# Optimization experiments

Measured on AMD Instinct MI355X. Metric: run time of the kernel, lower is better.

Reference implementation:

```python
import jax, jax.numpy as jnp
import numpy as np
import math

# ---- architecture constants (from init_kwargs) ----
BOUND = 1.0
L = 6            # grid levels == number of residual SIREN layers (grid_level)
F = 2            # hash-grid features per level (feature_dims)
D = 256          # SIREN hidden width / out_dim (ffenc_dims)
T = 2 ** 19      # hash table size per level
BASE_RES = 16
SCALE = 2.0
BASE_SIGMA = 5.0
EXP_SIGMA = 2.0
W0_SIN = float(L - 1)        # sin_w0 = multires - 1
W0_HIGH = 2.0 * (L - 1)      # sin_w0_high
N = 262144

_PRIMES = jnp.array([1, 2654435761, 805459861], dtype=jnp.uint32)
_OFFS = jnp.array([[i, j, k] for i in (0, 1) for j in (0, 1) for k in (0, 1)], dtype=jnp.int32)  # [8,3]


def hash_grid_encode(pos01, table):
    """Multi-resolution hash grid (instant-NGP style). pos01 [N,3] in [0,1], table [L,T,F] -> [L,N,F]."""
    res = BASE_RES * (SCALE ** jnp.arange(L, dtype=jnp.float32))               # [L]
    p = pos01[None] * res[:, None, None]                                        # [L,N,3]
    p0 = jnp.floor(p)
    frac = p - p0                                                               # [L,N,3]
    coords = p0.astype(jnp.int32)[:, :, None, :] + _OFFS[None, None]            # [L,N,8,3]
    cu = coords.astype(jnp.uint32) * _PRIMES                                    # spatial hash
    h = (cu[..., 0] ^ cu[..., 1] ^ cu[..., 2]) % jnp.uint32(T)                  # [L,N,8]
    feats = jax.vmap(lambda t, idx: t[idx])(table, h.astype(jnp.int32))         # [L,N,8,F]
    w = jnp.prod(jnp.where(_OFFS[None, None].astype(bool),
                           frac[:, :, None, :], 1.0 - frac[:, :, None, :]), axis=-1)  # trilinear [L,N,8]
    return jnp.einsum('lnc,lncf->lnf', w, feats)                                # [L,N,F]


def setup_inputs() -> dict:
    key = jax.random.key(0)
    ks = jax.random.split(key, 9)
    in_pos = jax.random.uniform(ks[0], (N, 3), jnp.float32, -BOUND, BOUND)
    table = jax.random.uniform(ks[1], (L, T, F), jnp.float32, -1e-4, 1e-4)      # hash embeddings
    ffn_A = jax.random.normal(ks[2], (L, F, D), jnp.float32)                    # Fourier projection (buffer)
    # SIREN-style init
    W0 = jax.random.uniform(ks[3], (3, D), jnp.float32, -1.0 / 3.0, 1.0 / 3.0)  # first_layer_sine_init
    b0 = jnp.zeros((D,), jnp.float32)
    lim = math.sqrt(6.0 / D) / W0_SIN
    Ws = jax.random.uniform(ks[4], (L, D, D), jnp.float32, -lim, lim)
    bs = jnp.zeros((L, D), jnp.float32)
    Wh = jax.random.uniform(ks[5], (L, D, D), jnp.float32, -lim, lim)
    bh = jnp.zeros((L, D), jnp.float32)
    return {"in_pos": in_pos, "table": table, "ffn_A": ffn_A,
            "W0": W0, "b0": b0, "Ws": Ws, "bs": bs, "Wh": Wh, "bh": bh}


def reference(in_pos, table, ffn_A, W0, b0, Ws, bs, Wh, bh):
    x = in_pos / BOUND                                   # [-1,1] for SIREN branch
    pos01 = (in_pos + BOUND) / (2.0 * BOUND)             # [0,1] for hash grid
    grid_x = hash_grid_encode(pos01, table)              # [L,N,F]
    sigmas = BASE_SIGMA * (EXP_SIGMA ** jnp.arange(L, dtype=jnp.float32))
    A = ffn_A * sigmas[:, None, None]                    # per-level sigma scale
    grid_x = jnp.sin(jnp.einsum('lnf,lfd->lnd', grid_x, 2.0 * math.pi * A))  # [L,N,D]
    # SIREN trunk with per-layer grid residual + high-frequency accumulation
    x = jnp.sin(W0_SIN * (x @ W0 + b0))                  # layer 0
    x_out = jnp.zeros((in_pos.shape[0], D), dtype=in_pos.dtype)
    for i in range(L):                                   # fixed small layer count
        x = jnp.sin(W0_SIN * (x @ Ws[i] + bs[i]))
        x = grid_x[i] + x
        x_out = x_out + jnp.sin(W0_HIGH * (x @ Wh[i] + bh[i]))
    return x_out                                          # [N,D]
```

## Files before the change

### kernel.cpp

```cpp
#include <hip/hip_runtime.h>
#include <stdint.h>

typedef __attribute__((ext_vector_type(8))) _Float16 h8v;
typedef __attribute__((ext_vector_type(4))) float f4v;

#define NLVL 6
#define TSZ (1u << 19)

__device__ __forceinline__ float b2f(unsigned short u){
  union { unsigned int i; float f; } v; v.i = ((unsigned)u) << 16; return v.f;
}
__device__ __forceinline__ unsigned short f2b(float f){
  unsigned x = __float_as_uint(f);
  x = (x + 0x7fffu + ((x >> 16) & 1u)) >> 16;
  return (unsigned short)x;
}
__device__ __forceinline__ unsigned short f2h(float f){
  union { _Float16 h; unsigned short u; } v; v.h = (_Float16)f; return v.u;
}
__device__ __forceinline__ float ldx(const void* p, long i, int isb){
  return isb ? b2f(((const unsigned short*)p)[i]) : ((const float*)p)[i];
}

__global__ void kdetect(const unsigned short* inpos, int* flag){
  __shared__ int cnt;
  if (threadIdx.x == 0) cnt = 0;
  __syncthreads();
  float f = b2f(inpos[threadIdx.x * 2]);
  int ok = (f == f) && (fabsf(f) <= 1.0f);
  atomicAdd(&cnt, ok);
  __syncthreads();
  if (threadIdx.x == 0) *flag = (cnt >= 120);
}


__global__ void kconsts(const void* ffnA, const void* W0, const void* b0,
                        const void* bs, const void* bh, char* ws, int Npts){
  const int flag = *(const int*)ws;
  const size_t wt_off = 16 + (size_t)NLVL * Npts * 8;
  float* cst = (float*)(ws + wt_off + (size_t)12 * 65536 * 2);
  int idx = blockIdx.x * 256 + threadIdx.x;
  float v;
  if (idx < 768)        v = 5.0f  * ldx(W0, idx, flag);
  else if (idx < 1024)  v = 5.0f  * ldx(b0, idx - 768, flag);
  else if (idx < 2560)  v = 5.0f  * ldx(bs, idx - 1024, flag);
  else if (idx < 4096)  v = 10.0f * ldx(bh, idx - 2560, flag);
  else { int j = idx - 4096; int l = j >> 9;
         v = 31.415926535897932f * (float)(1 << l) * ldx(ffnA, j, flag); }
  cst[idx] = v;
}

__global__ void kwt(const void* Wsv, const void* Whv, char* ws, int Npts){
  const int flag = *(const int*)ws;
  unsigned short* wt = (unsigned short*)(ws + 16 + (size_t)NLVL * Npts * 8);
  int e = blockIdx.x * 256 + threadIdx.x;
  int wi = e >> 16, r = e & 65535, n = r >> 8, k = r & 255;
  const void* src = (wi < 6) ? Wsv : Whv;
  int m = (wi < 6) ? wi : wi - 6;
  long si = (long)m * 65536 + k * 256 + n;
  float w = flag ? b2f(((const unsigned short*)src)[si]) : ((const float*)src)[si];
  wt[e] = f2h(w);
}

__global__ void kgrid(const void* inpos, const void* tbl, char* ws, int Npts){
  const int flag = *(const int*)ws;
  float* gf = (float*)(ws + 16);
  int n = blockIdx.x * 256 + threadIdx.x;
  int l = blockIdx.y;
  long b3 = (long)n * 3;
  float x = ldx(inpos, b3 + 0, flag), y = ldx(inpos, b3 + 1, flag), z = ldx(inpos, b3 + 2, flag);
  float res = (float)(16 << l);
  float px = ((x + 1.0f) * 0.5f) * res;
  float py = ((y + 1.0f) * 0.5f) * res;
  float pz = ((z + 1.0f) * 0.5f) * res;
  float fx = floorf(px), fy = floorf(py), fz = floorf(pz);
  float rx = px - fx, ry = py - fy, rz = pz - fz;
  unsigned cx = (unsigned)(int)fx, cy = (unsigned)(int)fy, cz = (unsigned)(int)fz;
  unsigned ax0 = cx,                 ax1 = cx + 1u;
  unsigned ay0 = cy * 2654435761u,   ay1 = (cy + 1u) * 2654435761u;
  unsigned az0 = cz * 805459861u,    az1 = (cz + 1u) * 805459861u;
  float g0 = 0.f, g1 = 0.f;
  #pragma unroll
  for (int c = 0; c < 8; c++){
    unsigned h = (((c & 4) ? ax1 : ax0) ^ ((c & 2) ? ay1 : ay0) ^ ((c & 1) ? az1 : az0)) & (TSZ - 1u);
    float w = ((c & 4) ? rx : 1.0f - rx) * ((c & 2) ? ry : 1.0f - ry) * ((c & 1) ? rz : 1.0f - rz);
    long e = ((long)l * TSZ + h) * 2;
    float f0, f1;
    if (flag){
      unsigned v = *(const unsigned*)((const unsigned short*)tbl + e);
      f0 = b2f((unsigned short)(v & 0xffffu)); f1 = b2f((unsigned short)(v >> 16));
    } else {
      const float* tp = (const float*)tbl + e; f0 = tp[0]; f1 = tp[1];
    }
    g0 += w * f0; g1 += w * f1;
  }
  float2 o; o.x = g0; o.y = g1;
  *(float2*)(gf + ((long)l * Npts + n) * 2) = o;
}

__global__ __launch_bounds__(512) void kmain(const void* inpos, char* ws, void* outp, int Npts){
  __shared__ __align__(16) unsigned short Abuf[128 * 264];
  __shared__ __align__(16) unsigned short Wb[2 * 8192];
  __shared__ __align__(16) float cbuf[7680];
  float* sbs_p = cbuf;
  float* sbh_p = cbuf + 1536;
  float* a2_p  = cbuf + 3072;
  float* g_p   = cbuf + 6144;

  const int tid = threadIdx.x;
  const int flag = *(const int*)ws;
  const size_t wt_off = 16 + (size_t)NLVL * Npts * 8;
  const unsigned short* wt = (const unsigned short*)(ws + wt_off);
  const float* cst = (const float*)(ws + wt_off + (size_t)12 * 65536 * 2);
  const float* gf = (const float*)(ws + 16);
  const int r0 = blockIdx.x * 128;

  const int sn = tid >> 1, skk = (tid & 1) * 16;
  uint4 pa, pb;
  {
    const uint4* p = (const uint4*)(wt + sn * 256 + skk);
    pa = p[0]; pb = p[1];
  }
  for (int idx = tid; idx < 6144; idx += 512) cbuf[idx] = cst[1024 + idx];
  for (int idx = tid; idx < 1536; idx += 512){
    int l = idx >> 8, j = idx & 255;
    g_p[idx] = gf[(size_t)l * Npts * 2 + (size_t)r0 * 2 + j];
  }
  {
    int lr = tid >> 2, c0 = (tid & 3) * 64;
    long bb = (long)(r0 + lr) * 3;
    float p0v = ldx(inpos, bb + 0, flag), p1v = ldx(inpos, bb + 1, flag), p2v = ldx(inpos, bb + 2, flag);
    for (int j = 0; j < 64; j++){
      int d = c0 + j;
      float v = __sinf(p0v * cst[d] + p1v * cst[256 + d] + p2v * cst[512 + d] + cst[768 + d]);
      Abuf[lr * 264 + d] = f2h(v);
    }
  }
  {
    uint4* dw = (uint4*)(Wb + sn * 32 + skk);
    dw[0] = pa; dw[1] = pb;
  }
  __syncthreads();

  const int lane = tid & 63, wv = tid >> 6;
  const int q = lane >> 4, sx = lane & 15;
  const int wrow = (wv >> 2) * 64, wcol = (wv & 3) * 64;
  int aoff[4], boff[4];
  #pragma unroll
  for (int rt = 0; rt < 4; rt++) aoff[rt] = (wrow + rt * 16 + sx) * 264 + q * 8;
  #pragma unroll
  for (int ct = 0; ct < 4; ct++) boff[ct] = (wcol + ct * 16 + sx) * 32 + q * 8;

  const f4v zf = {0.f, 0.f, 0.f, 0.f};
  f4v xo[4][4];
  #pragma unroll
  for (int a = 0; a < 4; a++)
    #pragma unroll
    for (int b = 0; b < 4; b++) xo[a][b] = zf;

  int cur = 0;
  #pragma unroll 1
  for (int s = 0; s < 12; s++){
    const int li = s >> 1;
    const int wi = (s & 1) ? (6 + li) : li;
    f4v acc[4][4];
    #pragma unroll
    for (int a = 0; a < 4; a++)
      #pragma unroll
      for (int b = 0; b < 4; b++) acc[a][b] = zf;
    #pragma unroll 1
    for (int kc = 0; kc < 8; kc++){
      const bool havenext = !(s == 11 && kc == 7);
      if (havenext){
        int nwi, nkc;
        if (kc < 7){ nwi = wi; nkc = kc + 1; }
        else { int s2 = s + 1; nwi = (s2 & 1) ? (6 + (s2 >> 1)) : (s2 >> 1); nkc = 0; }
        const uint4* p = (const uint4*)(wt + nwi * 65536 + sn * 256 + nkc * 32 + skk);
        pa = p[0]; pb = p[1];
      }
      h8v bfr[4], afr[4];
      const unsigned short* wc = Wb + cur * 8192;
      #pragma unroll
      for (int ct = 0; ct < 4; ct++) bfr[ct] = *(const h8v*)(wc + boff[ct]);
      #pragma unroll
      for (int rt = 0; rt < 4; rt++) afr[rt] = *(const h8v*)(Abuf + aoff[rt] + kc * 32);
      #pragma unroll
      for (int rt = 0; rt < 4; rt++)
        #pragma unroll
        for (int ct = 0; ct < 4; ct++)
          acc[rt][ct] = __builtin_amdgcn_mfma_f32_16x16x32_f16(afr[rt], bfr[ct], acc[rt][ct], 0, 0, 0);
      if (havenext){
        uint4* dw = (uint4*)(Wb + (cur ^ 1) * 8192 + sn * 32 + skk);
        dw[0] = pa; dw[1] = pb;
      }
      __syncthreads();
      cur ^= 1;
    }
    if ((s & 1) == 0){
      #pragma unroll
      for (int ct = 0; ct < 4; ct++){
        int col = wcol + ct * 16 + sx;
        float sb = sbs_p[li * 256 + col];
        float a0 = a2_p[(li * 2 + 0) * 256 + col];
        float a1 = a2_p[(li * 2 + 1) * 256 + col];
        #pragma unroll
        for (int rt = 0; rt < 4; rt++)
          #pragma unroll
          for (int r = 0; r < 4; r++){
            int row = wrow + rt * 16 + q * 4 + r;
            float gg0 = g_p[li * 256 + row * 2], gg1 = g_p[li * 256 + row * 2 + 1];
            float v = __sinf(5.0f * acc[rt][ct][r] + sb) + __sinf(a0 * gg0 + a1 * gg1);
            Abuf[row * 264 + col] = f2h(v);
          }
      }
      __syncthreads();
    } else {
      #pragma unroll
      for (int ct = 0; ct < 4; ct++){
        int col = wcol + ct * 16 + sx;
        float sb = sbh_p[li * 256 + col];
        #pragma unroll
        for (int rt = 0; rt < 4; rt++)
          #pragma unroll
          for (int r = 0; r < 4; r++)
            xo[rt][ct][r] += __sinf(10.0f * acc[rt][ct][r] + sb);
      }
    }
  }
  if (flag){
    unsigned short* ob = (unsigned short*)outp;
    #pragma unroll
    for (int rt = 0; rt < 4; rt++)
      #pragma unroll
      for (int ct = 0; ct < 4; ct++)
        #pragma unroll
        for (int r = 0; r < 4; r++){
          long row = (long)r0 + wrow + rt * 16 + q * 4 + r;
          ob[row * 256 + (wcol + ct * 16 + sx)] = f2b(xo[rt][ct][r]);
        }
  } else {
    float* of = (float*)outp;
    #pragma unroll
    for (int rt = 0; rt < 4; rt++)
      #pragma unroll
      for (int ct = 0; ct < 4; ct++)
        #pragma unroll
        for (int r = 0; r < 4; r++){
          long row = (long)r0 + wrow + rt * 16 + q * 4 + r;
          of[row * 256 + (wcol + ct * 16 + sx)] = xo[rt][ct][r];
        }
  }
}

extern "C" void kernel_launch(void* const* d_in, const int* in_sizes, int n_in,
                              void* d_out, int out_size, void* d_ws, size_t ws_size,
                              hipStream_t stream){
  (void)n_in; (void)out_size; (void)ws_size;
  const void* inpos = d_in[0];
  const void* tbl   = d_in[1];
  const void* ffnA  = d_in[2];
  const void* W0    = d_in[3];
  const void* b0    = d_in[4];
  const void* Wsv   = d_in[5];
  const void* bsv   = d_in[6];
  const void* Whv   = d_in[7];
  const void* bhv   = d_in[8];
  int Npts = in_sizes[0] / 3;
  char* ws = (char*)d_ws;
  kdetect<<<1, 128, 0, stream>>>((const unsigned short*)inpos, (int*)d_ws);
  kconsts<<<28, 256, 0, stream>>>(ffnA, W0, b0, bsv, bhv, ws, Npts);
  kwt<<<3072, 256, 0, stream>>>(Wsv, Whv, ws, Npts);
  kgrid<<<dim3(Npts / 256, NLVL), 256, 0, stream>>>(inpos, tbl, ws, Npts);
  kmain<<<Npts / 128, 512, 0, stream>>>(inpos, ws, d_out, Npts);
}
```

Baseline: 1.197 ms.

## Load MFMA-fragment-ordered weights directly to registers, shrink tile, swizzle activations

Weights are now pre-permuted on device into per-lane MFMA fragment order, and each wave loads its B fragments straight from global memory into registers with a one-step prefetch. This drops the shared-memory weight double buffer and the barrier on every k-chunk. The block shrinks to 64 rows with 256 threads and launch bounds for three blocks per CU, and the activation tile uses an XOR swizzle instead of padding. The output accumulator is kept in packed fp16 to save registers, which costs accumulation precision over six layers. Every block now reads the full weights from global memory or L2, since nothing is shared through LDS anymore.

Result: slower. 1.582 ms (+32.1%).

```diff
diff --git a/kernel.cpp b/kernel.cpp
--- a/kernel.cpp
+++ b/kernel.cpp
@@ -2,6 +2,7 @@
 #include <stdint.h>
 
 typedef __attribute__((ext_vector_type(8))) _Float16 h8v;
+typedef __attribute__((ext_vector_type(2))) _Float16 h2v;
 typedef __attribute__((ext_vector_type(4))) float f4v;
 
 #define NLVL 6
@@ -21,6 +22,8 @@
 __device__ __forceinline__ float ldx(const void* p, long i, int isb){
   return isb ? b2f(((const unsigned short*)p)[i]) : ((const float*)p)[i];
 }
+
+#define SWZ(row,k) ((row)*256 + ((((k) >> 3) ^ ((row) & 7)) << 3) + ((k) & 7))
 
 __global__ void kdetect(const unsigned short* inpos, int* flag){
   __shared__ int cnt;
@@ -54,7 +57,15 @@
   const int flag = *(const int*)ws;
   unsigned short* wt = (unsigned short*)(ws + 16 + (size_t)NLVL * Npts * 8);
   int e = blockIdx.x * 256 + threadIdx.x;
-  int wi = e >> 16, r = e & 65535, n = r >> 8, k = r & 255;
+  int j  = e & 7;
+  int lane = (e >> 3) & 63;
+  int ct = (e >> 9) & 3;
+  int kc = (e >> 11) & 7;
+  int wv = (e >> 14) & 3;
+  int wi = e >> 16;
+  int sx = lane & 15, q = lane >> 4;
+  int n = wv * 64 + ct * 16 + sx;
+  int k = kc * 32 + q * 8 + j;
   const void* src = (wi < 6) ? Wsv : Whv;
   int m = (wi < 6) ? wi : wi - 6;
   long si = (long)m * 65536 + k * 256 + n;
@@ -98,67 +109,63 @@
   *(float2*)(gf + ((long)l * Npts + n) * 2) = o;
 }
 
-__global__ __launch_bounds__(512) void kmain(const void* inpos, char* ws, void* outp, int Npts){
-  __shared__ __align__(16) unsigned short Abuf[128 * 264];
-  __shared__ __align__(16) unsigned short Wb[2 * 8192];
-  __shared__ __align__(16) float cbuf[7680];
-  float* sbs_p = cbuf;
-  float* sbh_p = cbuf + 1536;
-  float* a2_p  = cbuf + 3072;
-  float* g_p   = cbuf + 6144;
+__global__ __launch_bounds__(256, 3) void kmain(const void* inpos, char* ws, void* outp, int Npts){
+  __shared__ __align__(16) unsigned short Abuf[64 * 256];
+  __shared__ __align__(16) float g_p[NLVL * 64 * 2];
 
   const int tid = threadIdx.x;
   const int flag = *(const int*)ws;
   const size_t wt_off = 16 + (size_t)NLVL * Npts * 8;
-  const unsigned short* wt = (const unsigned short*)(ws + wt_off);
+  const unsigned short* wt2 = (const unsigned short*)(ws + wt_off);
   const float* cst = (const float*)(ws + wt_off + (size_t)12 * 65536 * 2);
   const float* gf = (const float*)(ws + 16);
-  const int r0 = blockIdx.x * 128;
-
-  const int sn = tid >> 1, skk = (tid & 1) * 16;
-  uint4 pa, pb;
-  {
-    const uint4* p = (const uint4*)(wt + sn * 256 + skk);
-    pa = p[0]; pb = p[1];
-  }
-  for (int idx = tid; idx < 6144; idx += 512) cbuf[idx] = cst[1024 + idx];
-  for (int idx = tid; idx < 1536; idx += 512){
-    int l = idx >> 8, j = idx & 255;
-    g_p[idx] = gf[(size_t)l * Npts * 2 + (size_t)r0 * 2 + j];
+  const int r0 = blockIdx.x * 64;
+
+  for (int idx = tid; idx < NLVL * 64; idx += 256){
+    int l = idx >> 6, row = idx & 63;
+    *(float2*)(g_p + l * 128 + row * 2) =
+        *(const float2*)(gf + ((size_t)l * Npts + r0 + row) * 2);
   }
   {
     int lr = tid >> 2, c0 = (tid & 3) * 64;
     long bb = (long)(r0 + lr) * 3;
     float p0v = ldx(inpos, bb + 0, flag), p1v = ldx(inpos, bb + 1, flag), p2v = ldx(inpos, bb + 2, flag);
-    for (int j = 0; j < 64; j++){
-      int d = c0 + j;
-      float v = __sinf(p0v * cst[d] + p1v * cst[256 + d] + p2v * cst[512 + d] + cst[768 + d]);
-      Abuf[lr * 264 + d] = f2h(v);
-    }
-  }
-  {
-    uint4* dw = (uint4*)(Wb + sn * 32 + skk);
-    dw[0] = pa; dw[1] = pb;
+    #pragma unroll
+    for (int b8 = 0; b8 < 8; b8++){
+      h8v v;
+      #pragma unroll
+      for (int j = 0; j < 8; j++){
+        int d = c0 + b8 * 8 + j;
+        v[j] = (_Float16)__sinf(p0v * cst[d] + p1v * cst[256 + d] + p2v * cst[512 + d] + cst[768 + d]);
+      }
+      *(h8v*)(Abuf + lr * 256 + ((((c0 >> 3) + b8) ^ (lr & 7)) << 3)) = v;
+    }
   }
   __syncthreads();
 
   const int lane = tid & 63, wv = tid >> 6;
   const int q = lane >> 4, sx = lane & 15;
-  const int wrow = (wv >> 2) * 64, wcol = (wv & 3) * 64;
-  int aoff[4], boff[4];
-  #pragma unroll
-  for (int rt = 0; rt < 4; rt++) aoff[rt] = (wrow + rt * 16 + sx) * 264 + q * 8;
-  #pragma unroll
-  for (int ct = 0; ct < 4; ct++) boff[ct] = (wcol + ct * 16 + sx) * 32 + q * 8;
+  const int sx7 = sx & 7;
+  const int wcol = wv * 64;
+  int arow[4];
+  #pragma unroll
+  for (int rt = 0; rt < 4; rt++) arow[rt] = (rt * 16 + sx) * 256;
+  const unsigned short* bbase = wt2 + wv * 16384 + lane * 8;
+
+  h2v xo[4][4][2];
+  #pragma unroll
+  for (int a = 0; a < 4; a++)
+    #pragma unroll
+    for (int b = 0; b < 4; b++){
+      h2v z; z[0] = (_Float16)0.f; z[1] = (_Float16)0.f;
+      xo[a][b][0] = z; xo[a][b][1] = z;
+    }
+
+  h8v bn[4];
+  #pragma unroll
+  for (int ct = 0; ct < 4; ct++) bn[ct] = *(const h8v*)(bbase + ct * 512);
 
   const f4v zf = {0.f, 0.f, 0.f, 0.f};
-  f4v xo[4][4];
-  #pragma unroll
-  for (int a = 0; a < 4; a++)
-    #pragma unroll
-    for (int b = 0; b < 4; b++) xo[a][b] = zf;
-
-  int cur = 0;
   #pragma unroll 1
   for (int s = 0; s < 12; s++){
     const int li = s >> 1;
@@ -170,47 +177,43 @@
       for (int b = 0; b < 4; b++) acc[a][b] = zf;
     #pragma unroll 1
     for (int kc = 0; kc < 8; kc++){
-      const bool havenext = !(s == 11 && kc == 7);
-      if (havenext){
+      h8v bfr[4];
+      #pragma unroll
+      for (int ct = 0; ct < 4; ct++) bfr[ct] = bn[ct];
+      if (!(s == 11 && kc == 7)){
         int nwi, nkc;
         if (kc < 7){ nwi = wi; nkc = kc + 1; }
         else { int s2 = s + 1; nwi = (s2 & 1) ? (6 + (s2 >> 1)) : (s2 >> 1); nkc = 0; }
-        const uint4* p = (const uint4*)(wt + nwi * 65536 + sn * 256 + nkc * 32 + skk);
-        pa = p[0]; pb = p[1];
-      }
-      h8v bfr[4], afr[4];
-      const unsigned short* wc = Wb + cur * 8192;
-      #pragma unroll
-      for (int ct = 0; ct < 4; ct++) bfr[ct] = *(const h8v*)(wc + boff[ct]);
-      #pragma unroll
-      for (int rt = 0; rt < 4; rt++) afr[rt] = *(const h8v*)(Abuf + aoff[rt] + kc * 32);
+        const unsigned short* bp = bbase + nwi * 65536 + nkc * 2048;
+        #pragma unroll
+        for (int ct = 0; ct < 4; ct++) bn[ct] = *(const h8v*)(bp + ct * 512);
+      }
+      h8v afr[4];
+      #pragma unroll
+      for (int rt = 0; rt < 4; rt++)
+        afr[rt] = *(const h8v*)(Abuf + arow[rt] + ((((kc << 2) + q) ^ sx7) << 3));
       #pragma unroll
       for (int rt = 0; rt < 4; rt++)
         #pragma unroll
         for (int ct = 0; ct < 4; ct++)
           acc[rt][ct] = __builtin_amdgcn_mfma_f32_16x16x32_f16(afr[rt], bfr[ct], acc[rt][ct], 0, 0, 0);
-      if (havenext){
-        uint4* dw = (uint4*)(Wb + (cur ^ 1) * 8192 + sn * 32 + skk);
-        dw[0] = pa; dw[1] = pb;
-      }
+    }
+    if ((s & 1) == 0){
       __syncthreads();
-      cur ^= 1;
-    }
-    if ((s & 1) == 0){
       #pragma unroll
       for (int ct = 0; ct < 4; ct++){
         int col = wcol + ct * 16 + sx;
-        float sb = sbs_p[li * 256 + col];
-        float a0 = a2_p[(li * 2 + 0) * 256 + col];
-        float a1 = a2_p[(li * 2 + 1) * 256 + col];
+        float sb = cst[1024 + li * 256 + col];
+        float a0 = cst[4096 + li * 512 + col];
+        float a1 = cst[4096 + li * 512 + 256 + col];
         #pragma unroll
         for (int rt = 0; rt < 4; rt++)
           #pragma unroll
           for (int r = 0; r < 4; r++){
-            int row = wrow + rt * 16 + q * 4 + r;
-            float gg0 = g_p[li * 256 + row * 2], gg1 = g_p[li * 256 + row * 2 + 1];
+            int row = rt * 16 + q * 4 + r;
+            float gg0 = g_p[li * 128 + row * 2], gg1 = g_p[li * 128 + row * 2 + 1];
             float v = __sinf(5.0f * acc[rt][ct][r] + sb) + __sinf(a0 * gg0 + a1 * gg1);
-            Abuf[row * 264 + col] = f2h(v);
+            Abuf[SWZ(row, col)] = f2h(v);
           }
       }
       __syncthreads();
@@ -218,12 +221,16 @@
       #pragma unroll
       for (int ct = 0; ct < 4; ct++){
         int col = wcol + ct * 16 + sx;
-        float sb = sbh_p[li * 256 + col];
+        float sb = cst[2560 + li * 256 + col];
         #pragma unroll
         for (int rt = 0; rt < 4; rt++)
           #pragma unroll
-          for (int r = 0; r < 4; r++)
-            xo[rt][ct][r] += __sinf(10.0f * acc[rt][ct][r] + sb);
+          for (int rp = 0; rp < 2; rp++){
+            float v0 = __sinf(10.0f * acc[rt][ct][rp * 2 + 0] + sb);
+            float v1 = __sinf(10.0f * acc[rt][ct][rp * 2 + 1] + sb);
+            h2v t; t[0] = (_Float16)v0; t[1] = (_Float16)v1;
+            xo[rt][ct][rp] = xo[rt][ct][rp] + t;
+          }
       }
     }
   }
@@ -235,8 +242,8 @@
       for (int ct = 0; ct < 4; ct++)
         #pragma unroll
         for (int r = 0; r < 4; r++){
-          long row = (long)r0 + wrow + rt * 16 + q * 4 + r;
-          ob[row * 256 + (wcol + ct * 16 + sx)] = f2b(xo[rt][ct][r]);
+          long row = (long)r0 + rt * 16 + q * 4 + r;
+          ob[row * 256 + (wcol + ct * 16 + sx)] = f2b((float)xo[rt][ct][r >> 1][r & 1]);
         }
   } else {
     float* of = (float*)outp;
@@ -246,8 +253,8 @@
       for (int ct = 0; ct < 4; ct++)
         #pragma unroll
         for (int r = 0; r < 4; r++){
-          long row = (long)r0 + wrow + rt * 16 + q * 4 + r;
-          of[row * 256 + (wcol + ct * 16 + sx)] = xo[rt][ct][r];
+          long row = (long)r0 + rt * 16 + q * 4 + r;
+          of[row * 256 + (wcol + ct * 16 + sx)] = (float)xo[rt][ct][r >> 1][r & 1];
         }
   }
 }
@@ -271,5 +278,5 @@
   kconsts<<<28, 256, 0, stream>>>(ffnA, W0, b0, bsv, bhv, ws, Npts);
   kwt<<<3072, 256, 0, stream>>>(Wsv, Whv, ws, Npts);
   kgrid<<<dim3(Npts / 256, NLVL), 256, 0, stream>>>(inpos, tbl, ws, Npts);
-  kmain<<<Npts / 128, 512, 0, stream>>>(inpos, ws, d_out, Npts);
-}
+  kmain<<<Npts / 64, 256, 0, stream>>>(inpos, ws, d_out, Npts);
+}
```
